# Kernel tuning notes

Hardware: AMD Instinct MI355X
Metric: run time of the kernel (lower is better)

The kernel has to match this reference:

```python
import jax, jax.numpy as jnp
import numpy as np

N = 100000        # unique nodes in batch (node_num)
IN_DIM = 256
OUT_DIM = 128
E_RAND = 1_600_000  # random graph edges (avg degree 16)
B = N             # batch nodes (all nodes, each gets a self-loop edge)
SLOPE = 0.1       # leaky_relu slope_ratio


def setup_inputs() -> dict:
    key = jax.random.key(0)
    k1, k2, k3, k4, k5, k6 = jax.random.split(key, 6)
    x = jax.random.normal(k1, (N, IN_DIM), dtype=jnp.float32)
    # small weight scale keeps exp(leaky_relu(.)) in a sane range, like kaiming on unit-ish inputs
    W = jax.random.normal(k2, (OUT_DIM, IN_DIM), dtype=jnp.float32) * 0.05
    b = jax.random.normal(k3, (OUT_DIM,), dtype=jnp.float32) * 0.05
    a = jax.random.normal(k4, (2 * OUT_DIM, 1), dtype=jnp.float32) * 0.05
    src = jax.random.randint(k5, (E_RAND,), 0, N, dtype=jnp.int32)
    dst = jax.random.randint(k6, (E_RAND,), 0, N, dtype=jnp.int32)
    batch_idx = jnp.arange(B, dtype=jnp.int32)
    # append self-loop edges for every batch node (original vstacks original_node_edge)
    edges = jnp.stack([jnp.concatenate([src, batch_idx]),
                       jnp.concatenate([dst, batch_idx])], axis=1)  # [E_TOT, 2]
    return {"x": x, "W": W, "b": b, "a": a, "edges": edges, "batch_idx": batch_idx}


def reference(x, W, b, a, edges, batch_idx):
    # new_embeddings = Linear(in_dim -> out_dim)
    emb = x @ W.T + b  # [N, out_dim]
    # concat(h_src, h_dst) @ a  ==  h_src @ a[:d] + h_dst @ a[d:]
    a1 = a[:OUT_DIM, 0]
    a2 = a[OUT_DIM:, 0]
    s_src = emb @ a1  # [N]
    s_dst = emb @ a2  # [N]
    src, dst = edges[:, 0], edges[:, 1]
    logits = s_src[src] + s_dst[dst]                                 # [E]
    score = jnp.exp(jax.nn.leaky_relu(logits, negative_slope=SLOPE))  # [E]
    # sparse row-sum and aggregation fused as segment reductions over src
    row_sum = jax.ops.segment_sum(score, src, num_segments=N)        # [N]
    msgs = score[:, None] * emb[dst]                                 # [E, out_dim]
    results = jax.ops.segment_sum(msgs, src, num_segments=N)         # [N, out_dim]
    # nodes with no outgoing edges have row_sum==0; they are never gathered below
    safe_rs = jnp.where(row_sum > 0, row_sum, 1.0)
    out = results / safe_rs[:, None]
    return out[batch_idx]
```

## Files before the change

### kernel.cpp

```cpp
#include <hip/hip_runtime.h>
#include <hip/hip_fp16.h>

#define IN_DIM 256
#define OUT_DIM 128
#define SLOPE 0.1f

typedef __attribute__((ext_vector_type(8))) short short8;
typedef __attribute__((ext_vector_type(4))) float f32x4;

__device__ __forceinline__ unsigned bf16_rne(float f) {
    unsigned u = __float_as_uint(f);
    return (u + 0x7FFFu + ((u >> 16) & 1u)) >> 16;
}

__global__ __launch_bounds__(256) void wsplit_kernel(
    const float* __restrict__ W, short* __restrict__ Whi, short* __restrict__ Wlo)
{
    const int i = blockIdx.x * 256 + threadIdx.x;
    const float v = W[i];
    const unsigned hb = bf16_rne(v);
    const float hf = __uint_as_float(hb << 16);
    Whi[i] = (short)hb;
    Wlo[i] = (short)bf16_rne(v - hf);
}

__global__ __launch_bounds__(256) void gemm_rank_kernel(
    const float* __restrict__ x, const short* __restrict__ Whi_g,
    const short* __restrict__ Wlo_g, const float* __restrict__ bias,
    const float* __restrict__ a, __half* __restrict__ emb_h,
    float* __restrict__ s1, float* __restrict__ s2,
    const int* __restrict__ edges, int* __restrict__ deg,
    int* __restrict__ rank, int N, int E, int nRank)
{
    __shared__ short lds[12288];

    if ((int)blockIdx.x < nRank) {
        const int e0 = ((int)blockIdx.x * 256 + (int)threadIdx.x) * 4;
        if (e0 + 3 < E) {
            const int4 ea = ((const int4*)edges)[(e0 >> 1) + 0];
            const int4 eb = ((const int4*)edges)[(e0 >> 1) + 1];
            const int r0 = atomicAdd(&deg[ea.x], 1);
            const int r1 = atomicAdd(&deg[ea.z], 1);
            const int r2 = atomicAdd(&deg[eb.x], 1);
            const int r3 = atomicAdd(&deg[eb.z], 1);
            ((int4*)rank)[e0 >> 2] = make_int4(r0, r1, r2, r3);
        } else if (e0 < E) {
            for (int e = e0; e < E; ++e) {
                const int2 ed = ((const int2*)edges)[e];
                rank[e] = atomicAdd(&deg[ed.x], 1);
            }
        }
        return;
    }

    short* Ahi = lds;
    short* Alo = lds + 2048;
    short* Bhi = lds + 4096;
    short* Blo = lds + 8192;

    const int tid = threadIdx.x;
    const int l   = tid & 63;
    const int w   = tid >> 6;
    const int gm0 = ((int)blockIdx.x - nRank) * 64;

    const int arow = tid >> 2;
    const int akc  = tid & 3;
    const int gmA  = gm0 + arow;
    const bool av_ok = (gmA < N);
    const int brow = tid >> 1;
    const int bkc0 = (tid & 1) * 2;

    f32x4 acc[8];
    #pragma unroll
    for (int j = 0; j < 8; ++j) acc[j] = (f32x4)0.f;

    float bias_v[8], av1[8], av2[8];
    #pragma unroll
    for (int nf = 0; nf < 8; ++nf) {
        const int col = nf * 16 + (l & 15);
        bias_v[nf] = bias[col];
        av1[nf]    = a[col];
        av2[nf]    = a[OUT_DIM + col];
    }

    for (int ks = 0; ks < 8; ++ks) {
        const int k0 = ks * 32;
        {
            float v[8];
            if (av_ok) {
                const float4 p0 = *(const float4*)&x[(size_t)gmA * IN_DIM + k0 + akc * 8];
                const float4 p1 = *(const float4*)&x[(size_t)gmA * IN_DIM + k0 + akc * 8 + 4];
                v[0]=p0.x; v[1]=p0.y; v[2]=p0.z; v[3]=p0.w;
                v[4]=p1.x; v[5]=p1.y; v[6]=p1.z; v[7]=p1.w;
            } else {
                #pragma unroll
                for (int j = 0; j < 8; ++j) v[j] = 0.f;
            }
            short8 h8, l8;
            #pragma unroll
            for (int j = 0; j < 8; ++j) {
                unsigned hb = bf16_rne(v[j]);
                float hf = __uint_as_float(hb << 16);
                h8[j] = (short)hb;
                l8[j] = (short)bf16_rne(v[j] - hf);
            }
            *(short8*)&Ahi[akc * 512 + arow * 8] = h8;
            *(short8*)&Alo[akc * 512 + arow * 8] = l8;
        }
        #pragma unroll
        for (int q = 0; q < 2; ++q) {
            const int kc = bkc0 + q;
            const short8 h8 = *(const short8*)&Whi_g[brow * IN_DIM + k0 + kc * 8];
            const short8 l8 = *(const short8*)&Wlo_g[brow * IN_DIM + k0 + kc * 8];
            *(short8*)&Bhi[kc * 1024 + brow * 8] = h8;
            *(short8*)&Blo[kc * 1024 + brow * 8] = l8;
        }
        __syncthreads();

        const int arow_f = w * 16 + (l & 15);
        const int aoff   = (l >> 4) * 512 + arow_f * 8;
        const short8 ah = *(const short8*)&Ahi[aoff];
        const short8 al = *(const short8*)&Alo[aoff];
        #pragma unroll
        for (int nf = 0; nf < 8; ++nf) {
            const int col = nf * 16 + (l & 15);
            const int boff = (l >> 4) * 1024 + col * 8;
            const short8 bh = *(const short8*)&Bhi[boff];
            const short8 bl = *(const short8*)&Blo[boff];
            acc[nf] = __builtin_amdgcn_mfma_f32_16x16x32_bf16(ah, bh, acc[nf], 0, 0, 0);
            acc[nf] = __builtin_amdgcn_mfma_f32_16x16x32_bf16(al, bh, acc[nf], 0, 0, 0);
            acc[nf] = __builtin_amdgcn_mfma_f32_16x16x32_bf16(ah, bl, acc[nf], 0, 0, 0);
        }
        __syncthreads();
    }

    __half* hl = (__half*)lds;
    #pragma unroll
    for (int r = 0; r < 4; ++r) {
        const int lrow = w * 16 + (l >> 4) * 4 + r;
        float p1 = 0.f, p2 = 0.f;
        #pragma unroll
        for (int nf = 0; nf < 8; ++nf) {
            const float e = acc[nf][r] + bias_v[nf];
            p1 += e * av1[nf];
            p2 += e * av2[nf];
            hl[lrow * 144 + nf * 16 + (l & 15)] = __float2half(e);
        }
        p1 += __shfl_xor(p1, 1); p1 += __shfl_xor(p1, 2);
        p1 += __shfl_xor(p1, 4); p1 += __shfl_xor(p1, 8);
        p2 += __shfl_xor(p2, 1); p2 += __shfl_xor(p2, 2);
        p2 += __shfl_xor(p2, 4); p2 += __shfl_xor(p2, 8);
        const int gm = gm0 + lrow;
        if ((l & 15) == 0 && gm < N) { s1[gm] = p1; s2[gm] = p2; }
    }
    __syncthreads();
    #pragma unroll
    for (int i = 0; i < 4; ++i) {
        const int idx = i * 256 + tid;
        const int row = idx >> 4, seg = idx & 15;
        if (gm0 + row < N) {
            const uint4 u = *(const uint4*)&hl[row * 144 + seg * 8];
            ((uint4*)emb_h)[(size_t)(gm0 + row) * 16 + seg] = u;
        }
    }
}

__global__ __launch_bounds__(256) void scan1_kernel(
    const int* __restrict__ deg, int* __restrict__ off,
    int* __restrict__ bsum, int N)
{
    __shared__ int lds[256];
    const int t = threadIdx.x;
    const int base = blockIdx.x * 1024 + t * 4;
    int v[4];
    int ts = 0;
    #pragma unroll
    for (int j = 0; j < 4; ++j) {
        v[j] = (base + j < N) ? deg[base + j] : 0;
        ts += v[j];
    }
    lds[t] = ts;
    __syncthreads();
    for (int d = 1; d < 256; d <<= 1) {
        int xv = (t >= d) ? lds[t - d] : 0;
        __syncthreads();
        lds[t] += xv;
        __syncthreads();
    }
    int run = lds[t] - ts;
    #pragma unroll
    for (int j = 0; j < 4; ++j) {
        if (base + j < N) off[base + j] = run;
        run += v[j];
    }
    if (t == 255) bsum[blockIdx.x] = lds[255];
}

__global__ __launch_bounds__(256) void scan3_kernel(
    int* __restrict__ off, const int* __restrict__ bsum,
    const int* __restrict__ bidx, int* __restrict__ flag, int N, int E)
{
    __shared__ int red[256];
    const int t = threadIdx.x;
    const int chunk = (int)(blockIdx.x >> 2);
    int s = 0;
    for (int j = t; j < chunk; j += 256) s += bsum[j];
    red[t] = s;
    __syncthreads();
    #pragma unroll
    for (int d = 128; d > 0; d >>= 1) {
        if (t < d) red[t] += red[t + d];
        __syncthreads();
    }
    const int pref = red[0];
    const int i = blockIdx.x * 256 + t;
    if (i < N) {
        off[i] += pref;
        if (bidx[i] != i) atomicOr(flag, 1);
    }
    if (i == 0) off[N] = E;
}

__global__ __launch_bounds__(256) void fill_kernel(
    const int* __restrict__ edges, const int* __restrict__ off,
    const int* __restrict__ rank, int* __restrict__ csr, int E)
{
    const int e0 = (blockIdx.x * 256 + threadIdx.x) * 4;
    if (e0 + 3 < E) {
        const int4 ea = ((const int4*)edges)[(e0 >> 1) + 0];
        const int4 eb = ((const int4*)edges)[(e0 >> 1) + 1];
        const int4 rk = ((const int4*)rank)[e0 >> 2];
        csr[off[ea.x] + rk.x] = ea.y;
        csr[off[ea.z] + rk.y] = ea.w;
        csr[off[eb.x] + rk.z] = eb.y;
        csr[off[eb.z] + rk.w] = eb.w;
    } else if (e0 < E) {
        for (int e = e0; e < E; ++e) {
            const int2 ed = ((const int2*)edges)[e];
            csr[off[ed.x] + rank[e]] = ed.y;
        }
    }
}

__global__ __launch_bounds__(256) void agg_kernel(
    const int* __restrict__ off, const int* __restrict__ csr,
    const float* __restrict__ s1, const float* __restrict__ s2,
    const __half* __restrict__ emb_h, const int* __restrict__ flag,
    float* __restrict__ results, float* __restrict__ out, int N)
{
    __shared__ int2 sl[4][64];

    const int wid  = (int)((blockIdx.x * 256u + threadIdx.x) >> 6);
    const int lane = threadIdx.x & 63;
    const int wv   = threadIdx.x >> 6;
    if (wid >= N) return;
    const int eg = lane >> 4;
    const int cl = lane & 15;
    const int beg = off[wid];
    const int end = off[wid + 1];
    const float s1n = s1[wid];

    const float4* __restrict__ embrow = (const float4*)emb_h;
    int2* slot = &sl[wv][0];

    float av[8];
    #pragma unroll
    for (int k = 0; k < 8; ++k) av[k] = 0.f;
    float rsl = 0.f;

    for (int tile = beg; tile < end; tile += 64) {
        const int cnt = min(64, end - tile);
        int d = 0; float sc = 0.f;
        if (lane < cnt) {
            d = csr[tile + lane];
            const float ll = s1n + s2[d];
            sc = __expf(ll > 0.f ? ll : SLOPE * ll);
        }
        rsl += sc;
        slot[lane] = make_int2(d, __float_as_int(sc));
        __builtin_amdgcn_wave_barrier();
        for (int j0 = 0; j0 < cnt; j0 += 32) {
            const int nq = ((cnt - j0) + 3) >> 2;
            int dq[8]; float scq[8];
            #pragma unroll
            for (int q = 0; q < 8; ++q) {
                dq[q] = 0; scq[q] = 0.f;
                if (q < nq) {
                    const int2 p = slot[j0 + q * 4 + eg];
                    dq[q] = p.x; scq[q] = __int_as_float(p.y);
                }
            }
            float4 vq[8];
            #pragma unroll
            for (int q = 0; q < 8; ++q)
                if (q < nq) vq[q] = embrow[(size_t)dq[q] * 16 + cl];
            #pragma unroll
            for (int q = 0; q < 8; ++q) {
                if (q < nq) {
                    const __half* hp = reinterpret_cast<const __half*>(&vq[q]);
                    #pragma unroll
                    for (int k = 0; k < 8; ++k)
                        av[k] += scq[q] * __half2float(hp[k]);
                }
            }
        }
        __builtin_amdgcn_wave_barrier();
    }

    float rs = rsl;
    rs += __shfl_xor(rs, 1);  rs += __shfl_xor(rs, 2);
    rs += __shfl_xor(rs, 4);  rs += __shfl_xor(rs, 8);
    rs += __shfl_xor(rs, 16); rs += __shfl_xor(rs, 32);
    #pragma unroll
    for (int k = 0; k < 8; ++k) {
        av[k] += __shfl_xor(av[k], 16);
        av[k] += __shfl_xor(av[k], 32);
    }

    const float inv = 1.f / (rs > 0.f ? rs : 1.f);
    if (eg == 0) {
        float* dbuf = (*flag == 0) ? out : results;
        float4* rp = (float4*)&dbuf[(size_t)wid * 128 + cl * 8];
        rp[0] = make_float4(av[0] * inv, av[1] * inv, av[2] * inv, av[3] * inv);
        rp[1] = make_float4(av[4] * inv, av[5] * inv, av[6] * inv, av[7] * inv);
    }
}

__global__ __launch_bounds__(256) void gather_kernel(
    const float* __restrict__ results, const int* __restrict__ bidx,
    const int* __restrict__ flag, float* __restrict__ out, int N)
{
    if (*flag == 0) return;
    const unsigned i = blockIdx.x * 256u + threadIdx.x;
    if (i >= (unsigned)N * 32u) return;
    const unsigned n = i >> 5, c = i & 31;
    ((float4*)out)[i] = ((const float4*)results)[(size_t)bidx[n] * 32 + c];
}

extern "C" void kernel_launch(void* const* d_in, const int* in_sizes, int n_in,
                              void* d_out, int out_size, void* d_ws, size_t ws_size,
                              hipStream_t stream) {
    const float* x     = (const float*)d_in[0];
    const float* W     = (const float*)d_in[1];
    const float* b     = (const float*)d_in[2];
    const float* a     = (const float*)d_in[3];
    const int*   edges = (const int*)d_in[4];
    const int*   bidx  = (const int*)d_in[5];

    const int N = in_sizes[5];
    const int E = in_sizes[4] / 2;

    float*  results = (float*)d_ws;
    __half* emb_h   = (__half*)(results + (size_t)N * OUT_DIM);
    int*    rank    = (int*)(emb_h + (size_t)N * OUT_DIM);
    int*    csr     = rank + E;
    float*  s1      = (float*)(csr + E);
    float*  s2      = s1 + N;
    int*    deg     = (int*)(s2 + N);
    int*    flag    = deg + N;
    int*    off     = flag + 1;
    int*    bsum    = off + N + 1;
    short*  Whi     = (short*)(bsum + 256);
    short*  Wlo     = Whi + OUT_DIM * IN_DIM;

    hipMemsetAsync(deg, 0, (size_t)(N + 1) * sizeof(int), stream);

    wsplit_kernel<<<(OUT_DIM * IN_DIM) / 256, 256, 0, stream>>>(W, Whi, Wlo);

    const int nRank = (E / 4 + 255) / 256 + 1;
    const int nGemm = (N + 63) / 64;
    gemm_rank_kernel<<<nRank + nGemm, 256, 0, stream>>>(
        x, Whi, Wlo, b, a, emb_h, s1, s2, edges, deg, rank, N, E, nRank);

    const int nb = (N + 1023) / 1024;
    scan1_kernel<<<nb, 256, 0, stream>>>(deg, off, bsum, N);
    scan3_kernel<<<(N + 255) / 256, 256, 0, stream>>>(off, bsum, bidx, flag, N, E);

    const int gE4 = (E / 4 + 255) / 256 + 1;
    fill_kernel<<<gE4, 256, 0, stream>>>(edges, off, rank, csr, E);

    const unsigned aggThreads = (unsigned)N * 64u;
    agg_kernel<<<(aggThreads + 255u) / 256u, 256, 0, stream>>>(
        off, csr, s1, s2, emb_h, flag, results, (float*)d_out, N);

    const unsigned gatherThreads = (unsigned)N * 32u;
    gather_kernel<<<(gatherThreads + 255u) / 256u, 256, 0, stream>>>(
        results, bidx, flag, (float*)d_out, N);
}
```

Measured before the change: 220.2 us.

## Replace atomic-rank CSR build with two-pass bucketed counting sort

The CSR construction now groups edges into buckets of 1024 source nodes. A histogram pass is fused with the W split, a single-block scan builds bucket bases, the GEMM kernel's side blocks scatter edges into per-bucket staging with LDS-local cursors, and a per-bucket kernel builds local offsets and CSR in shared memory. This replaces per-edge global atomics on random degree counters and the separate scan and fill kernels with mostly LDS atomics and more local writes. The aggregation inner loop also uses v_fma_mix_f32 to fuse the half-to-float conversion with the FMA. In exchange, edges are read an extra time, the bucket-base scan runs serially in one thread, and the CSR order within a node is nondeterministic.

```diff
diff --git a/kernel.cpp b/kernel.cpp
--- a/kernel.cpp
+++ b/kernel.cpp
@@ -4,6 +4,7 @@
 #define IN_DIM 256
 #define OUT_DIM 128
 #define SLOPE 0.1f
+#define EPB 4096
 
 typedef __attribute__((ext_vector_type(8))) short short8;
 typedef __attribute__((ext_vector_type(4))) float f32x4;
@@ -13,41 +14,103 @@
     return (u + 0x7FFFu + ((u >> 16) & 1u)) >> 16;
 }
 
-__global__ __launch_bounds__(256) void wsplit_kernel(
-    const float* __restrict__ W, short* __restrict__ Whi, short* __restrict__ Wlo)
-{
-    const int i = blockIdx.x * 256 + threadIdx.x;
-    const float v = W[i];
-    const unsigned hb = bf16_rne(v);
-    const float hf = __uint_as_float(hb << 16);
-    Whi[i] = (short)hb;
-    Wlo[i] = (short)bf16_rne(v - hf);
-}
-
-__global__ __launch_bounds__(256) void gemm_rank_kernel(
+__global__ __launch_bounds__(256) void wsplit_pass0_kernel(
+    const float* __restrict__ W, short* __restrict__ Whi, short* __restrict__ Wlo,
+    const int* __restrict__ edges, int* __restrict__ bucket_cnt, int E, int K)
+{
+    __shared__ int hist[4096];
+    const int tid = threadIdx.x;
+    if ((int)blockIdx.x < 128) {
+        const int i = blockIdx.x * 256 + tid;
+        const float v = W[i];
+        const unsigned hb = bf16_rne(v);
+        const float hf = __uint_as_float(hb << 16);
+        Whi[i] = (short)hb;
+        Wlo[i] = (short)bf16_rne(v - hf);
+        return;
+    }
+    const int pb = (int)blockIdx.x - 128;
+    for (int t = tid; t < K; t += 256) hist[t] = 0;
+    __syncthreads();
+    const int e0 = pb * EPB;
+    #pragma unroll
+    for (int i = 0; i < EPB / 256; ++i) {
+        const int e = e0 + i * 256 + tid;
+        if (e < E) {
+            const int src = ((const int2*)edges)[e].x;
+            atomicAdd(&hist[src >> 10], 1);
+        }
+    }
+    __syncthreads();
+    for (int t = tid; t < K; t += 256)
+        if (hist[t]) atomicAdd(&bucket_cnt[t], hist[t]);
+}
+
+__global__ __launch_bounds__(256) void scan_ident_kernel(
+    const int* __restrict__ bucket_cnt, int* __restrict__ bucket_base,
+    int* __restrict__ gcursor, int* __restrict__ off,
+    const int* __restrict__ bidx, int* __restrict__ flag, int N, int E, int K)
+{
+    const int tid = threadIdx.x;
+    if (blockIdx.x == 0) {
+        __shared__ int sc[4098];
+        for (int t = tid; t < K; t += 256) sc[t] = bucket_cnt[t];
+        __syncthreads();
+        if (tid == 0) {
+            int run = 0;
+            for (int b = 0; b < K; ++b) { const int c = sc[b]; sc[b] = run; run += c; }
+            sc[K] = run;
+        }
+        __syncthreads();
+        for (int t = tid; t <= K; t += 256) {
+            bucket_base[t] = sc[t];
+            if (t < K) gcursor[t] = sc[t];
+        }
+        if (tid == 0) off[N] = E;
+    }
+    const int i = blockIdx.x * 256 + tid;
+    if (i < N && bidx[i] != i) atomicOr(flag, 1);
+}
+
+__global__ __launch_bounds__(256) void gemm_pass1_kernel(
     const float* __restrict__ x, const short* __restrict__ Whi_g,
     const short* __restrict__ Wlo_g, const float* __restrict__ bias,
     const float* __restrict__ a, __half* __restrict__ emb_h,
     float* __restrict__ s1, float* __restrict__ s2,
-    const int* __restrict__ edges, int* __restrict__ deg,
-    int* __restrict__ rank, int N, int E, int nRank)
+    const int* __restrict__ edges, int* __restrict__ gcursor,
+    int2* __restrict__ tmp, int N, int E, int K, int nP1)
 {
     __shared__ short lds[12288];
 
-    if ((int)blockIdx.x < nRank) {
-        const int e0 = ((int)blockIdx.x * 256 + (int)threadIdx.x) * 4;
-        if (e0 + 3 < E) {
-            const int4 ea = ((const int4*)edges)[(e0 >> 1) + 0];
-            const int4 eb = ((const int4*)edges)[(e0 >> 1) + 1];
-            const int r0 = atomicAdd(&deg[ea.x], 1);
-            const int r1 = atomicAdd(&deg[ea.z], 1);
-            const int r2 = atomicAdd(&deg[eb.x], 1);
-            const int r3 = atomicAdd(&deg[eb.z], 1);
-            ((int4*)rank)[e0 >> 2] = make_int4(r0, r1, r2, r3);
-        } else if (e0 < E) {
-            for (int e = e0; e < E; ++e) {
+    const int tid = threadIdx.x;
+
+    if ((int)blockIdx.x < nP1) {
+        int* hist  = (int*)lds;
+        int* baseL = hist + K;
+        int* curL  = baseL + K;
+        for (int t = tid; t < K; t += 256) { hist[t] = 0; curL[t] = 0; }
+        __syncthreads();
+        const int e0 = (int)blockIdx.x * EPB;
+        #pragma unroll
+        for (int i = 0; i < EPB / 256; ++i) {
+            const int e = e0 + i * 256 + tid;
+            if (e < E) {
+                const int src = ((const int2*)edges)[e].x;
+                atomicAdd(&hist[src >> 10], 1);
+            }
+        }
+        __syncthreads();
+        for (int t = tid; t < K; t += 256)
+            if (hist[t]) baseL[t] = atomicAdd(&gcursor[t], hist[t]);
+        __syncthreads();
+        #pragma unroll
+        for (int i = 0; i < EPB / 256; ++i) {
+            const int e = e0 + i * 256 + tid;
+            if (e < E) {
                 const int2 ed = ((const int2*)edges)[e];
-                rank[e] = atomicAdd(&deg[ed.x], 1);
+                const int b = ed.x >> 10;
+                const int s = atomicAdd(&curL[b], 1);
+                tmp[baseL[b] + s] = ed;
             }
         }
         return;
@@ -58,10 +121,9 @@
     short* Bhi = lds + 4096;
     short* Blo = lds + 8192;
 
-    const int tid = threadIdx.x;
     const int l   = tid & 63;
     const int w   = tid >> 6;
-    const int gm0 = ((int)blockIdx.x - nRank) * 64;
+    const int gm0 = ((int)blockIdx.x - nP1) * 64;
 
     const int arow = tid >> 2;
     const int akc  = tid & 3;
@@ -165,80 +227,51 @@
     }
 }
 
-__global__ __launch_bounds__(256) void scan1_kernel(
-    const int* __restrict__ deg, int* __restrict__ off,
-    int* __restrict__ bsum, int N)
-{
-    __shared__ int lds[256];
-    const int t = threadIdx.x;
-    const int base = blockIdx.x * 1024 + t * 4;
-    int v[4];
-    int ts = 0;
-    #pragma unroll
-    for (int j = 0; j < 4; ++j) {
-        v[j] = (base + j < N) ? deg[base + j] : 0;
-        ts += v[j];
-    }
-    lds[t] = ts;
+__global__ __launch_bounds__(256) void pass2_kernel(
+    const int2* __restrict__ tmp, const int* __restrict__ bucket_base,
+    int* __restrict__ off, int* __restrict__ csr, int N)
+{
+    __shared__ int cnt[1024];
+    __shared__ int cur[1024];
+    __shared__ int part[256];
+
+    const int tid = threadIdx.x;
+    const int b   = blockIdx.x;
+    const int v0  = b << 10;
+    const int nloc = min(1024, N - v0);
+    const int s0 = bucket_base[b];
+    const int s1 = bucket_base[b + 1];
+    const int cntE = s1 - s0;
+
+    for (int t = tid; t < 1024; t += 256) cnt[t] = 0;
+    __syncthreads();
+    for (int e = tid; e < cntE; e += 256)
+        atomicAdd(&cnt[tmp[s0 + e].x - v0], 1);
+    __syncthreads();
+
+    int v[4], ts = 0;
+    #pragma unroll
+    for (int j = 0; j < 4; ++j) { v[j] = cnt[tid * 4 + j]; ts += v[j]; }
+    part[tid] = ts;
     __syncthreads();
     for (int d = 1; d < 256; d <<= 1) {
-        int xv = (t >= d) ? lds[t - d] : 0;
-        __syncthreads();
-        lds[t] += xv;
-        __syncthreads();
-    }
-    int run = lds[t] - ts;
-    #pragma unroll
-    for (int j = 0; j < 4; ++j) {
-        if (base + j < N) off[base + j] = run;
-        run += v[j];
-    }
-    if (t == 255) bsum[blockIdx.x] = lds[255];
-}
-
-__global__ __launch_bounds__(256) void scan3_kernel(
-    int* __restrict__ off, const int* __restrict__ bsum,
-    const int* __restrict__ bidx, int* __restrict__ flag, int N, int E)
-{
-    __shared__ int red[256];
-    const int t = threadIdx.x;
-    const int chunk = (int)(blockIdx.x >> 2);
-    int s = 0;
-    for (int j = t; j < chunk; j += 256) s += bsum[j];
-    red[t] = s;
-    __syncthreads();
-    #pragma unroll
-    for (int d = 128; d > 0; d >>= 1) {
-        if (t < d) red[t] += red[t + d];
-        __syncthreads();
-    }
-    const int pref = red[0];
-    const int i = blockIdx.x * 256 + t;
-    if (i < N) {
-        off[i] += pref;
-        if (bidx[i] != i) atomicOr(flag, 1);
-    }
-    if (i == 0) off[N] = E;
-}
-
-__global__ __launch_bounds__(256) void fill_kernel(
-    const int* __restrict__ edges, const int* __restrict__ off,
-    const int* __restrict__ rank, int* __restrict__ csr, int E)
-{
-    const int e0 = (blockIdx.x * 256 + threadIdx.x) * 4;
-    if (e0 + 3 < E) {
-        const int4 ea = ((const int4*)edges)[(e0 >> 1) + 0];
-        const int4 eb = ((const int4*)edges)[(e0 >> 1) + 1];
-        const int4 rk = ((const int4*)rank)[e0 >> 2];
-        csr[off[ea.x] + rk.x] = ea.y;
-        csr[off[ea.z] + rk.y] = ea.w;
-        csr[off[eb.x] + rk.z] = eb.y;
-        csr[off[eb.z] + rk.w] = eb.w;
-    } else if (e0 < E) {
-        for (int e = e0; e < E; ++e) {
-            const int2 ed = ((const int2*)edges)[e];
-            csr[off[ed.x] + rank[e]] = ed.y;
-        }
+        int xv = (tid >= d) ? part[tid - d] : 0;
+        __syncthreads();
+        part[tid] += xv;
+        __syncthreads();
+    }
+    int run = part[tid] - ts;
+    #pragma unroll
+    for (int j = 0; j < 4; ++j) { cur[tid * 4 + j] = run; run += v[j]; }
+    __syncthreads();
+
+    for (int lid = tid; lid < nloc; lid += 256) off[v0 + lid] = s0 + cur[lid];
+    __syncthreads();
+
+    for (int e = tid; e < cntE; e += 256) {
+        const int2 ed = tmp[s0 + e];
+        const int sl = atomicAdd(&cur[ed.x - v0], 1);
+        csr[s0 + sl] = ed.y;
     }
 }
 
@@ -297,10 +330,14 @@
             #pragma unroll
             for (int q = 0; q < 8; ++q) {
                 if (q < nq) {
-                    const __half* hp = reinterpret_cast<const __half*>(&vq[q]);
+                    const unsigned* up = reinterpret_cast<const unsigned*>(&vq[q]);
                     #pragma unroll
-                    for (int k = 0; k < 8; ++k)
-                        av[k] += scq[q] * __half2float(hp[k]);
+                    for (int p = 0; p < 4; ++p) {
+                        asm("v_fma_mix_f32 %0, %1, %2, %0 op_sel:[0,0,0] op_sel_hi:[1,0,0]"
+                            : "+v"(av[2 * p]) : "v"(up[p]), "v"(scq[q]));
+                        asm("v_fma_mix_f32 %0, %1, %2, %0 op_sel:[1,0,0] op_sel_hi:[1,0,0]"
+                            : "+v"(av[2 * p + 1]) : "v"(up[p]), "v"(scq[q]));
+                    }
                 }
             }
         }
@@ -349,35 +386,38 @@
 
     const int N = in_sizes[5];
     const int E = in_sizes[4] / 2;
+    const int K = (N + 1023) >> 10;
 
     float*  results = (float*)d_ws;
     __half* emb_h   = (__half*)(results + (size_t)N * OUT_DIM);
-    int*    rank    = (int*)(emb_h + (size_t)N * OUT_DIM);
-    int*    csr     = rank + E;
+    int2*   tmp     = (int2*)(emb_h + (size_t)N * OUT_DIM);
+    int*    csr     = (int*)(tmp + E);
     float*  s1      = (float*)(csr + E);
     float*  s2      = s1 + N;
-    int*    deg     = (int*)(s2 + N);
-    int*    flag    = deg + N;
-    int*    off     = flag + 1;
-    int*    bsum    = off + N + 1;
-    short*  Whi     = (short*)(bsum + 256);
+    int*    off     = (int*)(s2 + N);
+    int*    bucket_cnt  = off + N + 1;
+    int*    flag        = bucket_cnt + K;
+    int*    bucket_base = flag + 1;
+    int*    gcursor     = bucket_base + K + 1;
+    short*  Whi     = (short*)(gcursor + K);
     short*  Wlo     = Whi + OUT_DIM * IN_DIM;
 
-    hipMemsetAsync(deg, 0, (size_t)(N + 1) * sizeof(int), stream);
-
-    wsplit_kernel<<<(OUT_DIM * IN_DIM) / 256, 256, 0, stream>>>(W, Whi, Wlo);
-
-    const int nRank = (E / 4 + 255) / 256 + 1;
+    hipMemsetAsync(bucket_cnt, 0, (size_t)(K + 1) * sizeof(int), stream);
+
+    const int nP = (E + EPB - 1) / EPB;
+
+    wsplit_pass0_kernel<<<128 + nP, 256, 0, stream>>>(
+        W, Whi, Wlo, edges, bucket_cnt, E, K);
+
+    const int nIdent = (N + 255) / 256;
+    scan_ident_kernel<<<nIdent, 256, 0, stream>>>(
+        bucket_cnt, bucket_base, gcursor, off, bidx, flag, N, E, K);
+
     const int nGemm = (N + 63) / 64;
-    gemm_rank_kernel<<<nRank + nGemm, 256, 0, stream>>>(
-        x, Whi, Wlo, b, a, emb_h, s1, s2, edges, deg, rank, N, E, nRank);
-
-    const int nb = (N + 1023) / 1024;
-    scan1_kernel<<<nb, 256, 0, stream>>>(deg, off, bsum, N);
-    scan3_kernel<<<(N + 255) / 256, 256, 0, stream>>>(off, bsum, bidx, flag, N, E);
-
-    const int gE4 = (E / 4 + 255) / 256 + 1;
-    fill_kernel<<<gE4, 256, 0, stream>>>(edges, off, rank, csr, E);
+    gemm_pass1_kernel<<<nP + nGemm, 256, 0, stream>>>(
+        x, Whi, Wlo, b, a, emb_h, s1, s2, edges, gcursor, tmp, N, E, K, nP);
+
+    pass2_kernel<<<K, 256, 0, stream>>>(tmp, bucket_base, off, csr, N);
 
     const unsigned aggThreads = (unsigned)N * 64u;
     agg_kernel<<<(aggThreads + 255u) / 256u, 256, 0, stream>>>(
```

Measured after the change: 192.6 us. -12.6%, faster.
